# Kernel tuning notes

Hardware: AMD Instinct MI355X
Metric: run time of the kernel (lower is better)

Reference implementation:

```python
import jax, jax.numpy as jnp
import numpy as np

B, D, H = 8192, 256, 512


def setup_inputs() -> dict:
    key = jax.random.key(0)
    ks = jax.random.split(key, 25)
    inp = {
        "x": jax.random.normal(ks[0], (B, D), jnp.float32),
        "h_t": jax.random.normal(ks[1], (B, H), jnp.float32),
        "h_s": jax.random.normal(ks[2], (B, H), jnp.float32),
        "c_t": jax.random.normal(ks[3], (B, H), jnp.float32),
        "c_s": jax.random.normal(ks[4], (B, H), jnp.float32),
    }
    names = ["Ui", "Wti", "Wsi", "bi", "Us", "Wts", "Wss", "bs",
             "Ut", "Wtt", "Wst", "bt", "Uo", "Wto", "Wso", "bo",
             "Uc", "Wtc", "Wsc", "bc"]
    shapes = {"U": (D, H), "W": (H, H), "b": (H,)}
    scale = 0.02  # keep activations in a sane range
    for i, n in enumerate(names):
        s = shapes["U"] if n[0] == "U" else (shapes["b"] if n[0] == "b" else shapes["W"])
        inp[n] = jax.random.normal(ks[5 + i], s, jnp.float32) * scale
    return inp


def reference(x, h_t, h_s, c_t, c_s,
              Ui, Wti, Wsi, bi, Us, Wts, Wss, bs,
              Ut, Wtt, Wst, bt, Uo, Wto, Wso, bo,
              Uc, Wtc, Wsc, bc):
    # Fuse the 15 small GEMMs into 3 concatenated GEMMs: [B,D]@[D,5H] etc.
    U = jnp.concatenate([Ui, Us, Ut, Uo, Uc], axis=1)      # [D, 5H]
    Wt = jnp.concatenate([Wti, Wts, Wtt, Wto, Wtc], axis=1)  # [H, 5H]
    Ws = jnp.concatenate([Wsi, Wss, Wst, Wso, Wsc], axis=1)  # [H, 5H]
    b = jnp.concatenate([bi, bs, bt, bo, bc])                # [5H]
    gates = x @ U + h_t @ Wt + h_s @ Ws + b                  # [B, 5H]
    g_i, g_fs, g_ft, g_o, g_c = jnp.split(gates, 5, axis=1)
    i_n = jax.nn.sigmoid(g_i)
    f_s_n = jax.nn.sigmoid(g_fs)
    f_t_n = jax.nn.sigmoid(g_ft)
    o_n = jax.nn.sigmoid(g_o)
    c_n = jnp.tanh(g_c)
    c_h = i_n * c_n + f_t_n * c_t + f_s_n * c_s
    h = o_n * jnp.tanh(c_h)
    return (h, c_h)
```

## Files before the change

### kernel.cpp

```cpp
#include <hip/hip_runtime.h>
#include <hip/hip_bf16.h>
#include <cstdint>
#include <cstddef>

#define B_  8192
#define D_  256
#define H_  512
#define K_  1280
#define N_  2560
#define NT_ 320

typedef short short8  __attribute__((ext_vector_type(8)));
typedef float f32x4   __attribute__((ext_vector_type(4)));
typedef float f32x16  __attribute__((ext_vector_type(16)));

__device__ __forceinline__ float sigf(float x)     { return 1.f / (1.f + __expf(-x)); }
__device__ __forceinline__ float tanhfast(float x) { return 1.f - 2.f / (__expf(2.f * x) + 1.f); }

struct WPtrs {
    const float* U[5];
    const float* Wt[5];
    const float* Ws[5];
};

__global__ void prep_kernel(const float* __restrict__ x, const float* __restrict__ ht,
                            const float* __restrict__ hs, WPtrs p,
                            __hip_bfloat16* __restrict__ A, __hip_bfloat16* __restrict__ WT) {
    __shared__ __hip_bfloat16 tile[64][66];
    int bid = blockIdx.x;
    if (bid < 5120) {
        int t = bid * 256 + threadIdx.x;
        int idx8 = t * 8;
        int b = idx8 / K_;
        int k = idx8 - b * K_;
        const float* src;
        if (k < D_)            src = x  + (size_t)b * D_ + k;
        else if (k < D_ + H_)  src = ht + (size_t)b * H_ + (k - D_);
        else                   src = hs + (size_t)b * H_ + (k - D_ - H_);
        f32x4 v0 = *(const f32x4*)(src);
        f32x4 v1 = *(const f32x4*)(src + 4);
        union { short8 s; __hip_bfloat16 h[8]; } o;
        o.h[0] = __float2bfloat16(v0[0]); o.h[1] = __float2bfloat16(v0[1]);
        o.h[2] = __float2bfloat16(v0[2]); o.h[3] = __float2bfloat16(v0[3]);
        o.h[4] = __float2bfloat16(v1[0]); o.h[5] = __float2bfloat16(v1[1]);
        o.h[6] = __float2bfloat16(v1[2]); o.h[7] = __float2bfloat16(v1[3]);
        *(short8*)(A + idx8) = o.s;
    } else {
        int bid2 = bid - 5120;
        int hblk = bid2 & 7;
        int kblk = (bid2 >> 3) % 20;
        int g    = bid2 / 160;
        int k0 = kblk * 64;
        int h0 = hblk * 64;
        const float* src; int kl0;
        if (k0 < 256)      { src = p.U[g];  kl0 = k0; }
        else if (k0 < 768) { src = p.Wt[g]; kl0 = k0 - 256; }
        else               { src = p.Ws[g]; kl0 = k0 - 768; }
        int tid = threadIdx.x;
        int tk = tid >> 6;
        int th = tid & 63;
        for (int r = 0; r < 16; ++r) {
            int kl = r * 4 + tk;
            tile[kl][th] = __float2bfloat16(src[(size_t)(kl0 + kl) * H_ + h0 + th]);
        }
        __syncthreads();
        for (int r = 0; r < 16; ++r) {
            int hl = r * 4 + tk;
            int h  = h0 + hl;
            int np = (h >> 5) * 160 + g * 32 + (h & 31);
            WT[(size_t)np * K_ + k0 + th] = tile[th][hl];
        }
    }
}

#define GLD16(gp, lp)                                                              \
    __builtin_amdgcn_global_load_lds(                                              \
        (const __attribute__((address_space(1))) unsigned int*)(gp),               \
        (__attribute__((address_space(3))) unsigned int*)(lp), 16, 0, 0)

__global__ __launch_bounds__(256, 2) void gemm_fused_kernel(
    const __hip_bfloat16* __restrict__ A, const __hip_bfloat16* __restrict__ WT,
    const float* __restrict__ ct, const float* __restrict__ cs,
    const float* __restrict__ bi, const float* __restrict__ bfs,
    const float* __restrict__ bft, const float* __restrict__ bo,
    const float* __restrict__ bc, float* __restrict__ out) {
    __shared__ alignas(16) unsigned short sA[2][128 * 32];
    __shared__ alignas(16) unsigned short sB[2][NT_ * 32];

    int tid = threadIdx.x;
    int m0 = blockIdx.x * 128;
    int n0 = blockIdx.y * NT_;
    int wid  = tid >> 6, lane = tid & 63;
    int wm   = wid >> 1;
    int wn   = wid & 1;
    int half = lane >> 5, l31 = lane & 31;

    int hg = blockIdx.y * 2 + wn;
    int h  = hg * 32 + l31;
    float Bi = bi[h], Bfs = bfs[h], Bft = bft[h], Bo = bo[h], Bc = bc[h];

    f32x16 acc[2][5];
#pragma unroll
    for (int i = 0; i < 2; ++i)
#pragma unroll
        for (int j = 0; j < 5; ++j)
            acc[i][j] = (f32x16)(0.f);

    const __hip_bfloat16* aSrc[2]; int aOff[2];
#pragma unroll
    for (int i = 0; i < 2; ++i) {
        int c = tid + 256 * i;
        int row = c >> 2, pos = c & 3;
        int kc = pos ^ ((row >> 1) & 3);
        aSrc[i] = A + (size_t)(m0 + row) * K_ + kc * 8;
        aOff[i] = c * 8;
    }
    const __hip_bfloat16* bSrc[5]; int bOff[5];
#pragma unroll
    for (int i = 0; i < 5; ++i) {
        int c = tid + 256 * i;
        int row = c >> 2, pos = c & 3;
        int kc = pos ^ ((row >> 1) & 3);
        bSrc[i] = WT + (size_t)(n0 + row) * K_ + kc * 8;
        bOff[i] = c * 8;
    }

    int arow[2], brow[5];
#pragma unroll
    for (int i = 0; i < 2; ++i) arow[i] = wm * 64 + i * 32 + l31;
#pragma unroll
    for (int j = 0; j < 5; ++j) brow[j] = wn * 160 + j * 32 + l31;

#pragma unroll
    for (int i = 0; i < 2; ++i) GLD16(aSrc[i], &sA[0][aOff[i]]);
#pragma unroll
    for (int i = 0; i < 5; ++i) GLD16(bSrc[i], &sB[0][bOff[i]]);
    __syncthreads();

    int cur = 0;
    for (int k0 = 0; k0 < K_; k0 += 32) {
        if (k0 + 32 < K_) {
            int nxt = cur ^ 1;
#pragma unroll
            for (int i = 0; i < 2; ++i) GLD16(aSrc[i] + k0 + 32, &sA[nxt][aOff[i]]);
#pragma unroll
            for (int i = 0; i < 5; ++i) GLD16(bSrc[i] + k0 + 32, &sB[nxt][bOff[i]]);
        }

#pragma unroll
        for (int ks = 0; ks < 2; ++ks) {
            short8 a[2], b[5];
#pragma unroll
            for (int i = 0; i < 2; ++i) {
                int pos = (ks * 2 + half) ^ ((arow[i] >> 1) & 3);
                a[i] = *(const short8*)(&sA[cur][arow[i] * 32 + pos * 8]);
            }
#pragma unroll
            for (int j = 0; j < 5; ++j) {
                int pos = (ks * 2 + half) ^ ((brow[j] >> 1) & 3);
                b[j] = *(const short8*)(&sB[cur][brow[j] * 32 + pos * 8]);
            }
            __builtin_amdgcn_s_setprio(1);
#pragma unroll
            for (int j = 0; j < 5; ++j)
#pragma unroll
                for (int i = 0; i < 2; ++i)
                    acc[i][j] = __builtin_amdgcn_mfma_f32_32x32x16_bf16(a[i], b[j], acc[i][j], 0, 0, 0);
            __builtin_amdgcn_s_setprio(0);
        }
        __syncthreads();
        cur ^= 1;
    }

#pragma unroll
    for (int i = 0; i < 2; ++i) {
        int rbase = m0 + wm * 64 + i * 32 + 4 * half;
#pragma unroll
        for (int r = 0; r < 16; ++r) {
            int row = rbase + (r & 3) + 8 * (r >> 2);
            size_t idx = (size_t)row * H_ + h;
            float i_n  = sigf(acc[i][0][r] + Bi);
            float fs_n = sigf(acc[i][1][r] + Bfs);
            float ft_n = sigf(acc[i][2][r] + Bft);
            float o_n  = sigf(acc[i][3][r] + Bo);
            float c_n  = tanhfast(acc[i][4][r] + Bc);
            float ch   = i_n * c_n + ft_n * ct[idx] + fs_n * cs[idx];
            out[idx] = o_n * tanhfast(ch);
            out[(size_t)B_ * H_ + idx] = ch;
        }
    }
}

struct AllW {
    const float* U[5];
    const float* Wt[5];
    const float* Ws[5];
    const float* bias[5];
};

__global__ __launch_bounds__(512) void fallback_kernel(const float* __restrict__ x,
                                                       const float* __restrict__ ht,
                                                       const float* __restrict__ hs,
                                                       const float* __restrict__ ct,
                                                       const float* __restrict__ cs,
                                                       AllW w, float* __restrict__ out) {
    __shared__ float arow[K_];
    int b = blockIdx.x;
    int h = threadIdx.x;
    for (int k = h; k < K_; k += 512) {
        float v;
        if (k < D_)           v = x[b * D_ + k];
        else if (k < D_ + H_) v = ht[b * H_ + k - D_];
        else                  v = hs[b * H_ + k - D_ - H_];
        arow[k] = v;
    }
    __syncthreads();
    float g[5];
    for (int gi = 0; gi < 5; ++gi) {
        float s = w.bias[gi][h];
        const float* U = w.U[gi];
        for (int k = 0; k < D_; ++k) s += arow[k] * U[(size_t)k * H_ + h];
        const float* Wt = w.Wt[gi];
        for (int k = 0; k < H_; ++k) s += arow[D_ + k] * Wt[(size_t)k * H_ + h];
        const float* Ws = w.Ws[gi];
        for (int k = 0; k < H_; ++k) s += arow[D_ + H_ + k] * Ws[(size_t)k * H_ + h];
        g[gi] = s;
    }
    int idx = b * H_ + h;
    float i_n = sigf(g[0]), fs_n = sigf(g[1]), ft_n = sigf(g[2]), o_n = sigf(g[3]);
    float c_n = tanhfast(g[4]);
    float ch  = i_n * c_n + ft_n * ct[idx] + fs_n * cs[idx];
    out[idx] = o_n * tanhfast(ch);
    out[(size_t)B_ * H_ + idx] = ch;
}

extern "C" void kernel_launch(void* const* d_in, const int* in_sizes, int n_in,
                              void* d_out, int out_size, void* d_ws, size_t ws_size,
                              hipStream_t stream) {
    const float* x  = (const float*)d_in[0];
    const float* ht = (const float*)d_in[1];
    const float* hs = (const float*)d_in[2];
    const float* ct = (const float*)d_in[3];
    const float* cs = (const float*)d_in[4];

    WPtrs wp;
    AllW  aw;
    const float* bias[5];
    for (int g = 0; g < 5; ++g) {
        wp.U[g]  = (const float*)d_in[5 + g * 4 + 0];
        wp.Wt[g] = (const float*)d_in[5 + g * 4 + 1];
        wp.Ws[g] = (const float*)d_in[5 + g * 4 + 2];
        bias[g]  = (const float*)d_in[5 + g * 4 + 3];
        aw.U[g] = wp.U[g]; aw.Wt[g] = wp.Wt[g]; aw.Ws[g] = wp.Ws[g]; aw.bias[g] = bias[g];
    }
    float* out = (float*)d_out;

    size_t szA = (size_t)B_ * K_ * 2;
    size_t szW = (size_t)N_ * K_ * 2;

    if (ws_size >= szA + szW) {
        __hip_bfloat16* Abf = (__hip_bfloat16*)d_ws;
        __hip_bfloat16* WT  = (__hip_bfloat16*)((char*)d_ws + szA);

        prep_kernel<<<5120 + 800, 256, 0, stream>>>(x, ht, hs, wp, Abf, WT);
        gemm_fused_kernel<<<dim3(B_ / 128, N_ / NT_), 256, 0, stream>>>(
            Abf, WT, ct, cs, bias[0], bias[1], bias[2], bias[3], bias[4], out);
    } else {
        fallback_kernel<<<B_, 512, 0, stream>>>(x, ht, hs, ct, cs, aw, out);
    }
}
```

Baseline: 239.9 us.

## Prefetch two stages ahead with explicit waitcnt and split prep kernel

The GEMM main loop now issues global-to-LDS loads two K-tiles ahead using the two LDS buffers. It replaces __syncthreads with explicit s_barrier and vmcnt waits so one stage of loads can stay in flight during compute. All LDS fragment reads for a tile are hoisted ahead of the MFMA block, with a sched_barrier fencing them off. The prep kernel is split into separate activation-cast and weight-transpose launches, which adds a launch but removes branch divergence by block. Getting the waitcnt/barrier ordering right is subtle, and a mistake would cause races on LDS buffer reuse.

```diff
diff --git a/kernel.cpp b/kernel.cpp
--- a/kernel.cpp
+++ b/kernel.cpp
@@ -23,53 +23,51 @@
     const float* Ws[5];
 };
 
-__global__ void prep_kernel(const float* __restrict__ x, const float* __restrict__ ht,
-                            const float* __restrict__ hs, WPtrs p,
-                            __hip_bfloat16* __restrict__ A, __hip_bfloat16* __restrict__ WT) {
+__global__ void prep_a_kernel(const float* __restrict__ x, const float* __restrict__ ht,
+                              const float* __restrict__ hs, __hip_bfloat16* __restrict__ A) {
+    int t = blockIdx.x * 256 + threadIdx.x;
+    int idx8 = t * 8;
+    int b = idx8 / K_;
+    int k = idx8 - b * K_;
+    const float* src;
+    if (k < D_)            src = x  + (size_t)b * D_ + k;
+    else if (k < D_ + H_)  src = ht + (size_t)b * H_ + (k - D_);
+    else                   src = hs + (size_t)b * H_ + (k - D_ - H_);
+    f32x4 v0 = *(const f32x4*)(src);
+    f32x4 v1 = *(const f32x4*)(src + 4);
+    union { short8 s; __hip_bfloat16 h[8]; } o;
+    o.h[0] = __float2bfloat16(v0[0]); o.h[1] = __float2bfloat16(v0[1]);
+    o.h[2] = __float2bfloat16(v0[2]); o.h[3] = __float2bfloat16(v0[3]);
+    o.h[4] = __float2bfloat16(v1[0]); o.h[5] = __float2bfloat16(v1[1]);
+    o.h[6] = __float2bfloat16(v1[2]); o.h[7] = __float2bfloat16(v1[3]);
+    *(short8*)(A + idx8) = o.s;
+}
+
+__global__ void prep_w_kernel(WPtrs p, __hip_bfloat16* __restrict__ WT) {
     __shared__ __hip_bfloat16 tile[64][66];
-    int bid = blockIdx.x;
-    if (bid < 5120) {
-        int t = bid * 256 + threadIdx.x;
-        int idx8 = t * 8;
-        int b = idx8 / K_;
-        int k = idx8 - b * K_;
-        const float* src;
-        if (k < D_)            src = x  + (size_t)b * D_ + k;
-        else if (k < D_ + H_)  src = ht + (size_t)b * H_ + (k - D_);
-        else                   src = hs + (size_t)b * H_ + (k - D_ - H_);
-        f32x4 v0 = *(const f32x4*)(src);
-        f32x4 v1 = *(const f32x4*)(src + 4);
-        union { short8 s; __hip_bfloat16 h[8]; } o;
-        o.h[0] = __float2bfloat16(v0[0]); o.h[1] = __float2bfloat16(v0[1]);
-        o.h[2] = __float2bfloat16(v0[2]); o.h[3] = __float2bfloat16(v0[3]);
-        o.h[4] = __float2bfloat16(v1[0]); o.h[5] = __float2bfloat16(v1[1]);
-        o.h[6] = __float2bfloat16(v1[2]); o.h[7] = __float2bfloat16(v1[3]);
-        *(short8*)(A + idx8) = o.s;
-    } else {
-        int bid2 = bid - 5120;
-        int hblk = bid2 & 7;
-        int kblk = (bid2 >> 3) % 20;
-        int g    = bid2 / 160;
-        int k0 = kblk * 64;
-        int h0 = hblk * 64;
-        const float* src; int kl0;
-        if (k0 < 256)      { src = p.U[g];  kl0 = k0; }
-        else if (k0 < 768) { src = p.Wt[g]; kl0 = k0 - 256; }
-        else               { src = p.Ws[g]; kl0 = k0 - 768; }
-        int tid = threadIdx.x;
-        int tk = tid >> 6;
-        int th = tid & 63;
-        for (int r = 0; r < 16; ++r) {
-            int kl = r * 4 + tk;
-            tile[kl][th] = __float2bfloat16(src[(size_t)(kl0 + kl) * H_ + h0 + th]);
-        }
-        __syncthreads();
-        for (int r = 0; r < 16; ++r) {
-            int hl = r * 4 + tk;
-            int h  = h0 + hl;
-            int np = (h >> 5) * 160 + g * 32 + (h & 31);
-            WT[(size_t)np * K_ + k0 + th] = tile[th][hl];
-        }
+    int bid2 = blockIdx.x;
+    int hblk = bid2 & 7;
+    int kblk = (bid2 >> 3) % 20;
+    int g    = bid2 / 160;
+    int k0 = kblk * 64;
+    int h0 = hblk * 64;
+    const float* src; int kl0;
+    if (k0 < 256)      { src = p.U[g];  kl0 = k0; }
+    else if (k0 < 768) { src = p.Wt[g]; kl0 = k0 - 256; }
+    else               { src = p.Ws[g]; kl0 = k0 - 768; }
+    int tid = threadIdx.x;
+    int tk = tid >> 6;
+    int th = tid & 63;
+    for (int r = 0; r < 16; ++r) {
+        int kl = r * 4 + tk;
+        tile[kl][th] = __float2bfloat16(src[(size_t)(kl0 + kl) * H_ + h0 + th]);
+    }
+    __syncthreads();
+    for (int r = 0; r < 16; ++r) {
+        int hl = r * 4 + tk;
+        int h  = h0 + hl;
+        int np = (h >> 5) * 160 + g * 32 + (h & 31);
+        WT[(size_t)np * K_ + k0 + th] = tile[th][hl];
     }
 }
 
@@ -125,51 +123,65 @@
         bOff[i] = c * 8;
     }
 
+#define STAGE(buf, koff)                                                \
+    do {                                                                \
+        _Pragma("unroll")                                               \
+        for (int i_ = 0; i_ < 2; ++i_)                                  \
+            GLD16(aSrc[i_] + (koff), &sA[buf][aOff[i_]]);               \
+        _Pragma("unroll")                                               \
+        for (int i_ = 0; i_ < 5; ++i_)                                  \
+            GLD16(bSrc[i_] + (koff), &sB[buf][bOff[i_]]);               \
+    } while (0)
+
     int arow[2], brow[5];
 #pragma unroll
     for (int i = 0; i < 2; ++i) arow[i] = wm * 64 + i * 32 + l31;
 #pragma unroll
     for (int j = 0; j < 5; ++j) brow[j] = wn * 160 + j * 32 + l31;
 
-#pragma unroll
-    for (int i = 0; i < 2; ++i) GLD16(aSrc[i], &sA[0][aOff[i]]);
-#pragma unroll
-    for (int i = 0; i < 5; ++i) GLD16(bSrc[i], &sB[0][bOff[i]]);
-    __syncthreads();
-
-    int cur = 0;
-    for (int k0 = 0; k0 < K_; k0 += 32) {
-        if (k0 + 32 < K_) {
-            int nxt = cur ^ 1;
-#pragma unroll
-            for (int i = 0; i < 2; ++i) GLD16(aSrc[i] + k0 + 32, &sA[nxt][aOff[i]]);
-#pragma unroll
-            for (int i = 0; i < 5; ++i) GLD16(bSrc[i] + k0 + 32, &sB[nxt][bOff[i]]);
-        }
-
+    STAGE(0, 0);
+    STAGE(1, 32);
+    asm volatile("s_waitcnt vmcnt(7)" ::: "memory");
+    __builtin_amdgcn_s_barrier();
+
+    const int nt = K_ / 32;
+#pragma unroll 2
+    for (int t = 0; t < nt; ++t) {
+        int cur = t & 1;
+        short8 a[2][2], b[5][2];
 #pragma unroll
         for (int ks = 0; ks < 2; ++ks) {
-            short8 a[2], b[5];
 #pragma unroll
             for (int i = 0; i < 2; ++i) {
                 int pos = (ks * 2 + half) ^ ((arow[i] >> 1) & 3);
-                a[i] = *(const short8*)(&sA[cur][arow[i] * 32 + pos * 8]);
+                a[i][ks] = *(const short8*)(&sA[cur][arow[i] * 32 + pos * 8]);
             }
 #pragma unroll
             for (int j = 0; j < 5; ++j) {
                 int pos = (ks * 2 + half) ^ ((brow[j] >> 1) & 3);
-                b[j] = *(const short8*)(&sB[cur][brow[j] * 32 + pos * 8]);
+                b[j][ks] = *(const short8*)(&sB[cur][brow[j] * 32 + pos * 8]);
             }
-            __builtin_amdgcn_s_setprio(1);
+        }
+        asm volatile("s_waitcnt lgkmcnt(0)" ::: "memory");
+        __builtin_amdgcn_sched_barrier(0);
+        __builtin_amdgcn_s_setprio(1);
+#pragma unroll
+        for (int ks = 0; ks < 2; ++ks)
 #pragma unroll
             for (int j = 0; j < 5; ++j)
 #pragma unroll
                 for (int i = 0; i < 2; ++i)
-                    acc[i][j] = __builtin_amdgcn_mfma_f32_32x32x16_bf16(a[i], b[j], acc[i][j], 0, 0, 0);
-            __builtin_amdgcn_s_setprio(0);
+                    acc[i][j] = __builtin_amdgcn_mfma_f32_32x32x16_bf16(a[i][ks], b[j][ks], acc[i][j], 0, 0, 0);
+        __builtin_amdgcn_s_setprio(0);
+
+        __builtin_amdgcn_s_barrier();
+        if (t + 2 < nt) {
+            STAGE(cur, (t + 2) * 32);
+            asm volatile("s_waitcnt vmcnt(7)" ::: "memory");
+        } else {
+            asm volatile("s_waitcnt vmcnt(0)" ::: "memory");
         }
-        __syncthreads();
-        cur ^= 1;
+        __builtin_amdgcn_s_barrier();
     }
 
 #pragma unroll
@@ -189,6 +201,7 @@
             out[(size_t)B_ * H_ + idx] = ch;
         }
     }
+#undef STAGE
 }
 
 struct AllW {
@@ -262,7 +275,8 @@
         __hip_bfloat16* Abf = (__hip_bfloat16*)d_ws;
         __hip_bfloat16* WT  = (__hip_bfloat16*)((char*)d_ws + szA);
 
-        prep_kernel<<<5120 + 800, 256, 0, stream>>>(x, ht, hs, wp, Abf, WT);
+        prep_a_kernel<<<5120, 256, 0, stream>>>(x, ht, hs, Abf);
+        prep_w_kernel<<<800, 256, 0, stream>>>(wp, WT);
         gemm_fused_kernel<<<dim3(B_ / 128, N_ / NT_), 256, 0, stream>>>(
             Abf, WT, ct, cs, bias[0], bias[1], bias[2], bias[3], bias[4], out);
     } else {
```

Measured after the change: 242.3 us. About the same (+1.0%).
